# Kernel optimization log

Hardware: AMD Instinct MI355X
Metric: run time of the kernel (lower is better)

Reference implementation:

```python
import jax, jax.numpy as jnp
import numpy as np

DIM = 2048
NUM_EXPERTS = 64
NUM_TOKENS = 32768
CAPACITY_FACTOR = 1.0
EPSILON = 1e-6


def setup_inputs() -> dict:
    key = jax.random.key(0)
    k1, k2 = jax.random.split(key)
    x = jax.random.normal(k1, (NUM_TOKENS, DIM), dtype=jnp.float32)
    # nn.Linear(dim, num_experts): weight init ~ U(-1/sqrt(dim), 1/sqrt(dim))
    bound = 1.0 / np.sqrt(DIM)
    w_gate = jax.random.uniform(k2, (DIM, NUM_EXPERTS), dtype=jnp.float32,
                                minval=-bound, maxval=bound)
    b_gate = jnp.zeros((NUM_EXPERTS,), dtype=jnp.float32)
    return {"x": x, "w_gate": w_gate, "b_gate": b_gate}


def reference(x, w_gate, b_gate):
    # gate_scores = softmax(x @ W + b), shape [N, E]
    logits = jnp.einsum("nd,de->ne", x, w_gate) + b_gate
    gate_scores = jax.nn.softmax(logits, axis=-1)

    capacity = int(CAPACITY_FACTOR * x.shape[0])  # static

    # top-1 mask via argmax (equivalent to topk(1) + scatter of ones)
    top1 = jnp.argmax(gate_scores, axis=-1)                      # [N]
    mask = jax.nn.one_hot(top1, gate_scores.shape[-1],
                          dtype=gate_scores.dtype)               # [N, E]
    masked = gate_scores * mask

    # column-wise normalization, scaled by capacity
    denom = masked.sum(axis=0, keepdims=True) + EPSILON          # [1, E]
    return masked / denom * capacity
```

## Files before the change

kernel.cpp:

```cpp
#include <hip/hip_runtime.h>
#include <hip/hip_bf16.h>

#define DIM   2048
#define NEXP  64
#define NTOK  32768
#define KC    32
#define NC    64
#define TB    64
#define NBLK  (NTOK / TB)
#define NSLOT 5
#define BB    12288
#define WFOFF 1024

typedef __attribute__((ext_vector_type(8))) short bf16x8;
typedef __attribute__((ext_vector_type(4))) float f32x4;

typedef __attribute__((address_space(1))) const void gvoid_t;
typedef __attribute__((address_space(3))) void lvoid_t;
#define GLDS16(g, l) __builtin_amdgcn_global_load_lds((gvoid_t*)(g), (lvoid_t*)(l), 16, 0, 0)

__device__ __forceinline__ float rne_split(float v, short& h) {
    __hip_bfloat16 hb = __float2bfloat16(v);
    h = __builtin_bit_cast(short, hb);
    return __bfloat162float(hb);
}

__device__ __forceinline__ void split8(const float4& a, const float4& b,
                                       bf16x8& H, bf16x8& M, bf16x8& L) {
    const float vs[8] = {a.x, a.y, a.z, a.w, b.x, b.y, b.z, b.w};
#pragma unroll
    for (int j = 0; j < 8; ++j) {
        short h, m, l;
        const float fh = rne_split(vs[j], h);
        const float e1 = vs[j] - fh;
        const float fm = rne_split(e1, m);
        const float e2 = e1 - fm;
        rne_split(e2, l);
        H[j] = h; M[j] = m; L[j] = l;
    }
}

__global__ __launch_bounds__(256)
void wsplit_kernel(const float* __restrict__ w, bf16x8* __restrict__ wf,
                   float* __restrict__ denom) {
    if (blockIdx.x == 0 && threadIdx.x < NEXP) denom[threadIdx.x] = 0.0f;
    const int tid  = blockIdx.x * 256 + threadIdx.x;
    const int lane = tid & 63;
    const int ni   = (tid >> 6) & 3;
    const int ks   = tid >> 8;
    const int n    = ni * 16 + (lane & 15);
    const int k0   = ks * KC + (lane >> 4) * 8;
    bf16x8 H, M, L;
#pragma unroll
    for (int j = 0; j < 8; ++j) {
        const float v = w[(size_t)(k0 + j) * NEXP + n];
        short h, m, l;
        const float fh = rne_split(v, h);
        const float e1 = v - fh;
        const float fm = rne_split(e1, m);
        rne_split(e1 - fm, l);
        H[j] = h; M[j] = m; L[j] = l;
    }
    wf[((size_t)(ks * 3 + 0) * 4 + ni) * 64 + lane] = H;
    wf[((size_t)(ks * 3 + 1) * 4 + ni) * 64 + lane] = M;
    wf[((size_t)(ks * 3 + 2) * 4 + ni) * 64 + lane] = L;
}

__global__ __launch_bounds__(256, 2)
void gate_kernel(const float* __restrict__ x, const bf16x8* __restrict__ wf,
                 const float* __restrict__ b, float* __restrict__ out,
                 float* __restrict__ denom)
{
    __shared__ __align__(16) char slab[NSLOT * BB];
    __shared__ float dlds[NEXP];

    const int tid  = threadIdx.x;
    const int lane = tid & 63;
    const int l15  = lane & 15;
    const int l4   = lane >> 4;
    const int wv   = tid >> 6;
    const int tok0 = blockIdx.x * TB;

    if (tid < NEXP) dlds[tid] = 0.0f;

    float bias[4];
#pragma unroll
    for (int ni = 0; ni < 4; ++ni) bias[ni] = b[ni * 16 + l15];

    const float* xr0 = x + (size_t)(tok0 + wv * 16 + l15) * DIM + l4 * 8;

#define LOADX(X, c) {                                                  \
    X[0] = *(const float4*)(xr0 + (size_t)(c) * KC);                   \
    X[1] = *(const float4*)(xr0 + (size_t)(c) * KC + 4); }

#define STAGE(slot, c) {                                               \
    const char* _src = (const char*)wf + (size_t)(c) * BB + tid * 16;  \
    char* _dst = slab + (size_t)(slot) * BB + tid * 16;                \
    GLDS16(_src, _dst);                                                \
    GLDS16(_src + 4096, _dst + 4096);                                  \
    GLDS16(_src + 8192, _dst + 8192); }

    f32x4 acc[4];
#pragma unroll
    for (int ni = 0; ni < 4; ++ni) acc[ni] = (f32x4){0.f, 0.f, 0.f, 0.f};

    float4 xa[2], xb[2];
    STAGE(0, 0)
    __builtin_amdgcn_sched_barrier(0);
    STAGE(1, 1)
    __builtin_amdgcn_sched_barrier(0);
    LOADX(xa, 0)
    __builtin_amdgcn_sched_barrier(0);
    STAGE(2, 2)
    __builtin_amdgcn_sched_barrier(0);
    LOADX(xb, 1)
    __builtin_amdgcn_sched_barrier(0);
    STAGE(3, 3)
    __builtin_amdgcn_sched_barrier(0);

#define ITER(c, scomp, sstage, XC) {                                   \
    asm volatile("s_waitcnt vmcnt(8)" ::: "memory");                   \
    __builtin_amdgcn_s_barrier();                                      \
    __builtin_amdgcn_sched_barrier(0);                                 \
    const bf16x8* _bl = (const bf16x8*)(slab + (size_t)(scomp) * BB);  \
    bf16x8 Bf[12];                                                     \
    _Pragma("unroll")                                                  \
    for (int _f = 0; _f < 12; ++_f) Bf[_f] = _bl[_f * 64 + lane];      \
    __builtin_amdgcn_sched_barrier(0);                                 \
    bf16x8 Ah, Am, Al;                                                 \
    split8(XC[0], XC[1], Ah, Am, Al);                                  \
    __builtin_amdgcn_sched_barrier(0);                                 \
    { const int _cx = ((c) + 2 < NC) ? (c) + 2 : NC - 1;               \
      LOADX(XC, _cx) }                                                 \
    __builtin_amdgcn_sched_barrier(0);                                 \
    { const int _cs = ((c) + 4 < NC) ? (c) + 4 : NC - 1;               \
      STAGE(sstage, _cs) }                                             \
    __builtin_amdgcn_sched_barrier(0);                                 \
    _Pragma("unroll")                                                  \
    for (int _ni = 0; _ni < 4; ++_ni) {                                \
        f32x4 _a = acc[_ni];                                           \
        _a = __builtin_amdgcn_mfma_f32_16x16x32_bf16(Ah, Bf[_ni],     _a, 0, 0, 0); \
        _a = __builtin_amdgcn_mfma_f32_16x16x32_bf16(Ah, Bf[4 + _ni], _a, 0, 0, 0); \
        _a = __builtin_amdgcn_mfma_f32_16x16x32_bf16(Am, Bf[_ni],     _a, 0, 0, 0); \
        _a = __builtin_amdgcn_mfma_f32_16x16x32_bf16(Ah, Bf[8 + _ni], _a, 0, 0, 0); \
        _a = __builtin_amdgcn_mfma_f32_16x16x32_bf16(Am, Bf[4 + _ni], _a, 0, 0, 0); \
        _a = __builtin_amdgcn_mfma_f32_16x16x32_bf16(Al, Bf[_ni],     _a, 0, 0, 0); \
        acc[_ni] = _a;                                                 \
    } }

    int scomp = 0, sstage = 4;
#pragma unroll 1
    for (int c = 0; c < NC; c += 2) {
        ITER(c, scomp, sstage, xa)
        if (++scomp == NSLOT) scomp = 0;
        if (++sstage == NSLOT) sstage = 0;
        ITER(c + 1, scomp, sstage, xb)
        if (++scomp == NSLOT) scomp = 0;
        if (++sstage == NSLOT) sstage = 0;
    }

    asm volatile("s_waitcnt vmcnt(0)" ::: "memory");
    __syncthreads();

#pragma unroll
    for (int r = 0; r < 4; ++r) {
        const float v0 = acc[0][r] + bias[0];
        const float v1 = acc[1][r] + bias[1];
        const float v2 = acc[2][r] + bias[2];
        const float v3 = acc[3][r] + bias[3];

        float lm = v0; int le = l15;
        if (v1 > lm) { lm = v1; le = l15 + 16; }
        if (v2 > lm) { lm = v2; le = l15 + 32; }
        if (v3 > lm) { lm = v3; le = l15 + 48; }
#pragma unroll
        for (int off = 1; off < 16; off <<= 1) {
            const float om = __shfl_xor(lm, off);
            const int   oe = __shfl_xor(le, off);
            if (om > lm || (om == lm && oe < le)) { lm = om; le = oe; }
        }
        float s = __expf(v0 - lm) + __expf(v1 - lm) +
                  __expf(v2 - lm) + __expf(v3 - lm);
#pragma unroll
        for (int off = 1; off < 16; off <<= 1) s += __shfl_xor(s, off);
        const float g = 1.0f / s;

        const int t = tok0 + wv * 16 + 4 * l4 + r;
        float* orow = out + (size_t)t * NEXP + l15;
        orow[0]  = (le == l15     ) ? g : 0.0f;
        orow[16] = (le == l15 + 16) ? g : 0.0f;
        orow[32] = (le == l15 + 32) ? g : 0.0f;
        orow[48] = (le == l15 + 48) ? g : 0.0f;
        if (l15 == 0) atomicAdd(&dlds[le], g);
    }

    __syncthreads();
    if (tid < NEXP) atomicAdd(&denom[tid], dlds[tid]);
}

__global__ __launch_bounds__(256)
void scale_kernel(float* __restrict__ out, const float* __restrict__ denom)
{
    __shared__ float sc[NEXP];
    if (threadIdx.x < NEXP)
        sc[threadIdx.x] = (float)NTOK / (denom[threadIdx.x] + 1e-6f);
    __syncthreads();

    const size_t i = (size_t)blockIdx.x * blockDim.x + threadIdx.x;
    float4 v = ((const float4*)out)[i];
    const int e0 = (int)((i * 4) & (NEXP - 1));
    v.x *= sc[e0]; v.y *= sc[e0 + 1]; v.z *= sc[e0 + 2]; v.w *= sc[e0 + 3];
    ((float4*)out)[i] = v;
}

extern "C" void kernel_launch(void* const* d_in, const int* in_sizes, int n_in,
                              void* d_out, int out_size, void* d_ws, size_t ws_size,
                              hipStream_t stream) {
    const float* x = (const float*)d_in[0];
    const float* w = (const float*)d_in[1];
    const float* b = (const float*)d_in[2];
    float*  out   = (float*)d_out;
    float*  denom = (float*)d_ws;
    bf16x8* wf    = (bf16x8*)((char*)d_ws + WFOFF);

    wsplit_kernel<<<64, 256, 0, stream>>>(w, wf, denom);
    gate_kernel<<<NBLK, 256, 0, stream>>>(x, wf, b, out, denom);
    scale_kernel<<<(NTOK * NEXP / 4) / 256, 256, 0, stream>>>(out, denom);
}
```

Before: 80.40 us.

## Fuse column-scale pass into gate kernel via cooperative grid sync

Removes the separate scale kernel. The gate kernel now keeps each token's gate value in registers, performs a grid-wide sync once all blocks have accumulated the per-expert denominators, and writes the final scaled output directly. This saves a full read-modify-write pass over the 8 MB output and one kernel launch. In exchange it requires a cooperative launch in which all 512 blocks are co-resident, and every block waits at a grid barrier.

```diff
diff --git a/kernel.cpp b/kernel.cpp
--- a/kernel.cpp
+++ b/kernel.cpp
@@ -1,5 +1,8 @@
 #include <hip/hip_runtime.h>
 #include <hip/hip_bf16.h>
+#include <hip/hip_cooperative_groups.h>
+
+namespace cg = cooperative_groups;
 
 #define DIM   2048
 #define NEXP  64
@@ -162,6 +165,7 @@
     asm volatile("s_waitcnt vmcnt(0)" ::: "memory");
     __syncthreads();
 
+    float gv[4]; int lev[4];
 #pragma unroll
     for (int r = 0; r < 4; ++r) {
         const float v0 = acc[0][r] + bias[0];
@@ -183,34 +187,30 @@
                   __expf(v2 - lm) + __expf(v3 - lm);
 #pragma unroll
         for (int off = 1; off < 16; off <<= 1) s += __shfl_xor(s, off);
-        const float g = 1.0f / s;
-
+        gv[r]  = 1.0f / s;
+        lev[r] = le;
+        if (l15 == 0) atomicAdd(&dlds[le], gv[r]);
+    }
+
+    __syncthreads();
+    if (tid < NEXP) atomicAdd(&denom[tid], dlds[tid]);
+
+    cg::this_grid().sync();
+
+    const float sc0 = (float)NTOK / (denom[l15]      + 1e-6f);
+    const float sc1 = (float)NTOK / (denom[l15 + 16] + 1e-6f);
+    const float sc2 = (float)NTOK / (denom[l15 + 32] + 1e-6f);
+    const float sc3 = (float)NTOK / (denom[l15 + 48] + 1e-6f);
+
+#pragma unroll
+    for (int r = 0; r < 4; ++r) {
         const int t = tok0 + wv * 16 + 4 * l4 + r;
         float* orow = out + (size_t)t * NEXP + l15;
-        orow[0]  = (le == l15     ) ? g : 0.0f;
-        orow[16] = (le == l15 + 16) ? g : 0.0f;
-        orow[32] = (le == l15 + 32) ? g : 0.0f;
-        orow[48] = (le == l15 + 48) ? g : 0.0f;
-        if (l15 == 0) atomicAdd(&dlds[le], g);
-    }
-
-    __syncthreads();
-    if (tid < NEXP) atomicAdd(&denom[tid], dlds[tid]);
-}
-
-__global__ __launch_bounds__(256)
-void scale_kernel(float* __restrict__ out, const float* __restrict__ denom)
-{
-    __shared__ float sc[NEXP];
-    if (threadIdx.x < NEXP)
-        sc[threadIdx.x] = (float)NTOK / (denom[threadIdx.x] + 1e-6f);
-    __syncthreads();
-
-    const size_t i = (size_t)blockIdx.x * blockDim.x + threadIdx.x;
-    float4 v = ((const float4*)out)[i];
-    const int e0 = (int)((i * 4) & (NEXP - 1));
-    v.x *= sc[e0]; v.y *= sc[e0 + 1]; v.z *= sc[e0 + 2]; v.w *= sc[e0 + 3];
-    ((float4*)out)[i] = v;
+        orow[0]  = (lev[r] == l15     ) ? gv[r] * sc0 : 0.0f;
+        orow[16] = (lev[r] == l15 + 16) ? gv[r] * sc1 : 0.0f;
+        orow[32] = (lev[r] == l15 + 32) ? gv[r] * sc2 : 0.0f;
+        orow[48] = (lev[r] == l15 + 48) ? gv[r] * sc3 : 0.0f;
+    }
 }
 
 extern "C" void kernel_launch(void* const* d_in, const int* in_sizes, int n_in,
@@ -224,6 +224,8 @@
     bf16x8* wf    = (bf16x8*)((char*)d_ws + WFOFF);
 
     wsplit_kernel<<<64, 256, 0, stream>>>(w, wf, denom);
-    gate_kernel<<<NBLK, 256, 0, stream>>>(x, wf, b, out, denom);
-    scale_kernel<<<(NTOK * NEXP / 4) / 256, 256, 0, stream>>>(out, denom);
-}
+
+    void* args[] = {(void*)&x, (void*)&wf, (void*)&b, (void*)&out, (void*)&denom};
+    hipLaunchCooperativeKernel((void*)gate_kernel, dim3(NBLK), dim3(256),
+                               args, 0, stream);
+}
```

Result: slower. 161.0 us (+100.2%).
